# Kernel optimization log

Measured on AMD Instinct MI355X. Metric: run time of the kernel, lower is better.

Reference implementation:

```python
import jax, jax.numpy as jnp
import numpy as np

DN = ('NCHW', 'OIHW', 'NCHW')
B, H, W = 2048, 16, 16
DICT, SE, CE, ESZ, NZ = 14, 8, 16, 512, 512
EPS = 1e-4


def _conv(x, w, b):
    # 3x3 conv, padding=1 (SAME), NCHW
    return jax.lax.conv_general_dilated(x, w, (1, 1), 'SAME', dimension_numbers=DN) + b[None, :, None, None]


def _normalized(m, eps=0.0):
    return m / (jnp.sqrt(jnp.sum(m * m, axis=1, keepdims=True)) + eps)


def setup_inputs() -> dict:
    key = jax.random.key(0)
    ks = jax.random.split(key, 20)
    f = jnp.float32
    d = {
        's': jax.random.randint(ks[0], (B, H, W), 0, DICT, dtype=jnp.int32),
        's_prime': jax.random.randint(ks[1], (B, H, W), 0, DICT, dtype=jnp.int32),
        'state_embed': jax.random.normal(ks[2], (DICT, SE), f),
        'conv_embed_w': jax.random.normal(ks[3], (CE, SE, 3, 3), f) * 0.1,
        'conv_embed_b': jnp.zeros((CE,), f),
        'p1c1_w': jax.random.normal(ks[4], (16, CE, 3, 3), f) * 0.1,
        'p1c1_b': jnp.zeros((16,), f),
        'p1c2_w': jax.random.normal(ks[5], (32, 16, 3, 3), f) * 0.1,
        'p1c2_b': jnp.zeros((32,), f),
        'p1l_w': jax.random.normal(ks[6], (ESZ, 32 * H * W), f) * 0.02,
        'p1l_b': jnp.zeros((ESZ,), f),
        'p2c1_w': jax.random.normal(ks[7], (16, CE, 3, 3), f) * 0.1,
        'p2c1_b': jnp.zeros((16,), f),
        'p2c2_w': jax.random.normal(ks[8], (32, 16, 3, 3), f) * 0.1,
        'p2c2_b': jnp.zeros((32,), f),
        'p2l_w': jax.random.normal(ks[9], (ESZ, 32 * H * W), f) * 0.02,
        'p2l_b': jnp.zeros((ESZ,), f),
        'z_vectors': jax.random.normal(ks[10], (NZ, ESZ), f),
        'scale': jnp.ones((1,), f),
        'downscale_factor': 1,
    }
    return d


def _embed(s, state_embed, conv_embed_w, conv_embed_b):
    # nn.Embedding(max_norm=1): renorm rows to L2 norm <= 1 before lookup
    norms = jnp.sqrt(jnp.sum(state_embed * state_embed, axis=1, keepdims=True))
    table = state_embed / jnp.maximum(norms, 1.0)
    x = table[s]  # (B, H, W, SE)
    x = jnp.transpose(x, (0, 3, 1, 2))  # (B, SE, H, W)
    return _conv(x, conv_embed_w, conv_embed_b)


def _tower(x, c1w, c1b, c2w, c2b, lw, lb):
    x = jax.nn.relu(_conv(x, c1w, c1b))
    x = jax.nn.relu(_conv(x, c2w, c2b))
    x = x.reshape(x.shape[0], -1)  # (B, 32*H*W)
    x = x @ lw.T + lb
    return _normalized(x, EPS)


def reference(s, s_prime, state_embed, conv_embed_w, conv_embed_b,
              p1c1_w, p1c1_b, p1c2_w, p1c2_b, p1l_w, p1l_b,
              p2c1_w, p2c1_b, p2c2_w, p2c2_b, p2l_w, p2l_b,
              z_vectors, scale, downscale_factor):
    s_e = _embed(s, state_embed, conv_embed_w, conv_embed_b)
    sp_e = _embed(s_prime, state_embed, conv_embed_w, conv_embed_b)
    embed1 = _tower(s_e, p1c1_w, p1c1_b, p1c2_w, p1c2_b, p1l_w, p1l_b)
    embed2 = _tower(sp_e - s_e, p2c1_w, p2c1_b, p2c2_w, p2c2_b, p2l_w, p2l_b)
    # VQ: cosine-similarity nearest codebook vector
    zn = _normalized(z_vectors, 0.0)  # (NZ, ESZ)
    z_inds = jnp.argmax(embed2 @ zn.T, axis=1)  # (B,)
    z_matrix = zn[z_inds]  # (B, ESZ)
    if downscale_factor == 1:
        ipm = embed1 @ z_matrix.T  # (B, B)
    else:
        bs = embed1.shape[0] // downscale_factor
        v1 = embed1[::downscale_factor]  # (bs, ESZ)
        v2 = z_matrix.reshape(bs, downscale_factor, -1)
        ipm = jnp.einsum('be,bde->bd', v1, v2)
    return jnp.exp(scale) * ipm
```

## Files before the change

kernel.cpp:

```cpp
#include <hip/hip_runtime.h>
#include <math.h>


typedef __attribute__((ext_vector_type(8))) __bf16 bf16x8;
typedef __attribute__((ext_vector_type(4))) float f32x4;
typedef __attribute__((ext_vector_type(8))) unsigned short ushort8;
typedef __attribute__((ext_vector_type(4))) unsigned short ushort4v;

static __device__ __forceinline__ unsigned short f2bf(float x) {
  union { float f; unsigned u; } v; v.f = x;
  return (unsigned short)(v.u >> 16);
}
static __device__ __forceinline__ float bf2f(unsigned short h) {
  union { float f; unsigned u; } v; v.u = ((unsigned)h) << 16;
  return v.f;
}
template<int NS>
static __device__ __forceinline__ void split3(float x, unsigned short* h) {
  unsigned short q0 = f2bf(x); h[0] = q0;
  float r1 = x - bf2f(q0);
  unsigned short q1 = f2bf(r1); h[1] = q1;
  if constexpr (NS == 3) h[2] = f2bf(r1 - bf2f(q1));
}
static __device__ __forceinline__ void gload_lds16(const void* g, void* l) {
  __builtin_amdgcn_global_load_lds(
      (const __attribute__((address_space(1))) unsigned int*)g,
      (__attribute__((address_space(3))) unsigned int*)l, 16, 0, 0);
}
#define MFMA16(a, b, c) __builtin_amdgcn_mfma_f32_16x16x32_bf16((a), (b), (c), 0, 0, 0)

template<int NS>
static __device__ __forceinline__ f32x4 mfma_prod(const bf16x8* a, const bf16x8* b, f32x4 c) {
  c = MFMA16(a[0], b[0], c);
  c = MFMA16(a[0], b[1], c);
  c = MFMA16(a[1], b[0], c);
  if constexpr (NS == 3) {
    c = MFMA16(a[1], b[1], c);
    c = MFMA16(a[0], b[2], c);
    c = MFMA16(a[2], b[0], c);
  }
  return c;
}
static __device__ __forceinline__ int conv_a16(int cell, int half) {
  return (cell * 2 + half) ^ ((cell >> 2) & 7);
}
static __device__ __forceinline__ unsigned long long score_key(float v, int col) {
  unsigned b = __float_as_uint(v);
  unsigned m = b ^ ((unsigned)((int)b >> 31) | 0x80000000u);
  return ((unsigned long long)m << 32) | (unsigned)(511 - col);
}
static __device__ __forceinline__ unsigned long long shfl_xor_u64(unsigned long long v, int m) {
  unsigned lo = __shfl_xor((unsigned)v, m, 64);
  unsigned hi = __shfl_xor((unsigned)(v >> 32), m, 64);
  return ((unsigned long long)hi << 32) | lo;
}

__global__ __launch_bounds__(256) void prep_misc_kernel(
    const float* __restrict__ se, float* __restrict__ tbl,
    const float* __restrict__ zv,
    unsigned short* __restrict__ zn0, unsigned short* __restrict__ zn1,
    unsigned short* __restrict__ zn2,
    float* __restrict__ epre, unsigned long long* __restrict__ zi)
{
  __shared__ float wsum[4];
  const int b = blockIdx.x, t = threadIdx.x;
  if (b == 0) {
    if (t < 112) {
      int r = t >> 3;
      float ss = 0.f;
      #pragma unroll
      for (int i = 0; i < 8; ++i) { float v = se[r * 8 + i]; ss += v * v; }
      float n = fmaxf(sqrtf(ss), 1.0f);
      tbl[t] = se[t] / n;
    }
  } else if (b <= 512) {
    int row = b - 1;
    size_t base = (size_t)row * 512 + t * 2;
    float2 v = *reinterpret_cast<const float2*>(zv + base);
    float ss = v.x * v.x + v.y * v.y;
    #pragma unroll
    for (int m = 32; m >= 1; m >>= 1) ss += __shfl_xor(ss, m, 64);
    int lane = t & 63, wid = t >> 6;
    if (lane == 0) wsum[wid] = ss;
    __syncthreads();
    float tot = wsum[0] + wsum[1] + wsum[2] + wsum[3];
    float inv = 1.0f / sqrtf(tot);
    float a = v.x * inv, c = v.y * inv;
    unsigned short ha[3], hc[3];
    split3<3>(a, ha); split3<3>(c, hc);
    zn0[base] = ha[0]; zn0[base + 1] = hc[0];
    zn1[base] = ha[1]; zn1[base + 1] = hc[1];
    zn2[base] = ha[2]; zn2[base + 1] = hc[2];
  } else if (b <= 1024) {
    f32x4 z4 = {0.f, 0.f, 0.f, 0.f};
    size_t o = ((size_t)(b - 513) * 256 + t) * 8;
    *reinterpret_cast<f32x4*>(epre + o) = z4;
    *reinterpret_cast<f32x4*>(epre + o + 4) = z4;
  } else {
    int i = (b - 1025) * 256 + t;
    if (i < 2048) zi[i] = 0ull;
  }
}

__global__ __launch_bounds__(256) void prep_wt_all_kernel(
    const float* __restrict__ ew,
    const float* __restrict__ p1c1w, const float* __restrict__ p1c2w,
    const float* __restrict__ p2c1w, const float* __restrict__ p2c2w,
    unsigned short* __restrict__ wt)
{
  int gi = blockIdx.x * 256 + threadIdx.x;
  if (gi >= 50688) return;
  const float* src; int off, NSs, OC, mode;
  if (gi < 4608)       { src = ew;    off = 0;     NSs = 3; OC = 16; mode = 0; }
  else if (gi < 12288) { src = p1c1w; off = 4608;  NSs = 5; OC = 16; mode = 1; }
  else if (gi < 27648) { src = p1c2w; off = 12288; NSs = 5; OC = 32; mode = 1; }
  else if (gi < 35328) { src = p2c1w; off = 27648; NSs = 5; OC = 16; mode = 1; }
  else                 { src = p2c2w; off = 35328; NSs = 5; OC = 32; mode = 1; }
  int i = gi - off;
  int ic = i & 7;
  int r = i >> 3;
  int oc = r % OC; r /= OC;
  int kc = r & 3; r >>= 2;
  int s = r % NSs;
  int sp = r / NSs;
  int tap, icf, IC;
  if (mode == 0) { tap = s * 4 + kc; icf = ic; IC = 8; }
  else           { tap = s * 2 + (kc >> 1); icf = (kc & 1) * 8 + ic; IC = 16; }
  float w = 0.f;
  if (tap < 9) {
    int ky = tap / 3, kx = tap - ky * 3;
    w = src[((oc * IC + icf) * 3 + ky) * 3 + kx];
  }
  unsigned short h[3];
  split3<3>(w, h);
  wt[gi] = h[sp];
}

__global__ __launch_bounds__(256) void reduce_norm_kernel(
    const float* __restrict__ pre, const float* __restrict__ bias, float eps,
    unsigned short* __restrict__ o0, unsigned short* __restrict__ o1,
    unsigned short* __restrict__ o2, float* __restrict__ zero_dst)
{
  int row = blockIdx.x, t = threadIdx.x;
  size_t base = (size_t)row * 512 + t * 2;
  float2 v = *reinterpret_cast<const float2*>(pre + base);
  float ax = v.x + bias[t * 2], ay = v.y + bias[t * 2 + 1];
  float ss = ax * ax + ay * ay;
  #pragma unroll
  for (int m = 32; m >= 1; m >>= 1) ss += __shfl_xor(ss, m, 64);
  __shared__ float wsum[4];
  int lane = t & 63, wid = t >> 6;
  if (lane == 0) wsum[wid] = ss;
  __syncthreads();
  float tot = wsum[0] + wsum[1] + wsum[2] + wsum[3];
  float inv = 1.0f / (sqrtf(tot) + eps);
  float a = ax * inv, b2 = ay * inv;
  unsigned short ha[3], hb[3];
  split3<3>(a, ha); split3<3>(b2, hb);
  o0[base] = ha[0]; o0[base + 1] = hb[0];
  o1[base] = ha[1]; o1[base + 1] = hb[1];
  if (o2) { o2[base] = ha[2]; o2[base + 1] = hb[2]; }
  if (zero_dst) {
    float2 z = {0.f, 0.f};
    *reinterpret_cast<float2*>(zero_dst + base) = z;
  }
}

template<int NS>
__global__ __launch_bounds__(256) void tower_mfma_kernel(
    const int* __restrict__ sIdx, const int* __restrict__ spIdx,
    const float* __restrict__ tblf,
    const unsigned short* __restrict__ wtE,
    const unsigned short* __restrict__ wt1,
    const unsigned short* __restrict__ wt2,
    const float* __restrict__ eb, const float* __restrict__ c1b,
    const float* __restrict__ c2b,
    unsigned short* __restrict__ a0, unsigned short* __restrict__ a1,
    unsigned short* __restrict__ a2, int delta)
{
  __shared__ float tbl[112];
  __shared__ ushort8 G[NS][324];
  __shared__ ushort8 Abuf[NS][648];
  __shared__ ushort8 Bbuf[NS][648];

  const int b = blockIdx.x, t = threadIdx.x;
  const int lane = t & 63, wv = t >> 6;
  const int fr = lane & 15, kc = lane >> 4;

  if (t < 112) tbl[t] = tblf[t];
  if (t < 68) {
    int c;
    if (t < 18)      c = t;
    else if (t < 36) c = 306 + (t - 18);
    else if (t < 52) c = 18 * (t - 35);
    else             c = 18 * (t - 51) + 17;
    ushort8 z8 = {0, 0, 0, 0, 0, 0, 0, 0};
    #pragma unroll
    for (int sp = 0; sp < NS; ++sp) {
      G[sp][c] = z8;
      ((ushort8*)&Abuf[sp][0])[conv_a16(c, 0)] = z8;
      ((ushort8*)&Abuf[sp][0])[conv_a16(c, 1)] = z8;
      ((ushort8*)&Bbuf[sp][0])[conv_a16(c, 0)] = z8;
      ((ushort8*)&Bbuf[sp][0])[conv_a16(c, 1)] = z8;
    }
  }
  __syncthreads();

  {
    const int y = t >> 4, x = t & 15;
    const int cell = (y + 1) * 18 + (x + 1);
    int sv = sIdx[(size_t)b * 256 + t];
    float v[8];
    if (delta) {
      int spv = spIdx[(size_t)b * 256 + t];
      #pragma unroll
      for (int c = 0; c < 8; ++c) v[c] = tbl[spv * 8 + c] - tbl[sv * 8 + c];
    } else {
      #pragma unroll
      for (int c = 0; c < 8; ++c) v[c] = tbl[sv * 8 + c];
    }
    ushort8 h0, h1, h2;
    #pragma unroll
    for (int c = 0; c < 8; ++c) {
      unsigned short q[3];
      split3<NS>(v[c], q);
      h0[c] = q[0]; h1[c] = q[1];
      if constexpr (NS == 3) h2[c] = q[2];
    }
    G[0][cell] = h0; G[1][cell] = h1;
    if constexpr (NS == 3) G[2][cell] = h2;
  }
  __syncthreads();

  {
    float bias = 0.f;
    if (!delta) bias = eb[fr];
    f32x4 acc[4];
    #pragma unroll
    for (int j = 0; j < 4; ++j) acc[j] = (f32x4)0.f;
    #pragma unroll
    for (int s = 0; s < 3; ++s) {
      bf16x8 bw[NS];
      #pragma unroll
      for (int sp = 0; sp < NS; ++sp)
        bw[sp] = __builtin_bit_cast(bf16x8, *reinterpret_cast<const ushort8*>(
            wtE + (size_t)(((sp * 3 + s) * 4 + kc) * 16 + fr) * 8));
      int tap = s * 4 + kc; if (tap > 8) tap = 8;
      const int dy = tap / 3, dx = tap - dy * 3;
      const int cb = dy * 18 + fr + dx;
      #pragma unroll
      for (int j = 0; j < 4; ++j) {
        const int cell = cb + (wv * 4 + j) * 18;
        bf16x8 av[NS];
        #pragma unroll
        for (int sp = 0; sp < NS; ++sp)
          av[sp] = __builtin_bit_cast(bf16x8, G[sp][cell]);
        acc[j] = mfma_prod<NS>(av, bw, acc[j]);
      }
    }
    #pragma unroll
    for (int j = 0; j < 4; ++j) {
      const int y = wv * 4 + j;
      #pragma unroll
      for (int q = 0; q < 4; ++q) {
        const int x = kc * 4 + q;
        const int cell = (y + 1) * 18 + (x + 1);
        const int a16 = conv_a16(cell, fr >> 3);
        unsigned short hh[3];
        split3<NS>(acc[j][q] + bias, hh);
        #pragma unroll
        for (int sp = 0; sp < NS; ++sp)
          ((unsigned short*)&Abuf[sp][0])[a16 * 8 + (fr & 7)] = hh[sp];
      }
    }
  }
  __syncthreads();

  {
    const float bias = c1b[fr];
    f32x4 acc[4];
    #pragma unroll
    for (int j = 0; j < 4; ++j) acc[j] = (f32x4)0.f;
    #pragma unroll
    for (int s = 0; s < 5; ++s) {
      bf16x8 bw[NS];
      #pragma unroll
      for (int sp = 0; sp < NS; ++sp)
        bw[sp] = __builtin_bit_cast(bf16x8, *reinterpret_cast<const ushort8*>(
            wt1 + (size_t)(((sp * 5 + s) * 4 + kc) * 16 + fr) * 8));
      int tap = s * 2 + (kc >> 1); if (tap > 8) tap = 8;
      const int dy = tap / 3, dx = tap - dy * 3;
      const int half = kc & 1;
      const int cb = dy * 18 + fr + dx;
      #pragma unroll
      for (int j = 0; j < 4; ++j) {
        const int cell = cb + (wv * 4 + j) * 18;
        const int a16 = conv_a16(cell, half);
        bf16x8 av[NS];
        #pragma unroll
        for (int sp = 0; sp < NS; ++sp)
          av[sp] = __builtin_bit_cast(bf16x8, *reinterpret_cast<const ushort8*>(
              (const unsigned short*)&Abuf[sp][0] + a16 * 8));
        acc[j] = mfma_prod<NS>(av, bw, acc[j]);
      }
    }
    #pragma unroll
    for (int j = 0; j < 4; ++j) {
      const int y = wv * 4 + j;
      #pragma unroll
      for (int q = 0; q < 4; ++q) {
        const int x = kc * 4 + q;
        const int cell = (y + 1) * 18 + (x + 1);
        const int a16 = conv_a16(cell, fr >> 3);
        unsigned short hh[3];
        split3<NS>(fmaxf(acc[j][q] + bias, 0.f), hh);
        #pragma unroll
        for (int sp = 0; sp < NS; ++sp)
          ((unsigned short*)&Bbuf[sp][0])[a16 * 8 + (fr & 7)] = hh[sp];
      }
    }
  }
  __syncthreads();

  {
    const float bias0 = c2b[fr], bias1 = c2b[16 + fr];
    f32x4 acc0[4], acc1[4];
    #pragma unroll
    for (int j = 0; j < 4; ++j) { acc0[j] = (f32x4)0.f; acc1[j] = (f32x4)0.f; }
    #pragma unroll
    for (int s = 0; s < 5; ++s) {
      bf16x8 bw0[NS], bw1[NS];
      #pragma unroll
      for (int sp = 0; sp < NS; ++sp) {
        size_t base = (size_t)(((sp * 5 + s) * 4 + kc) * 32) * 8;
        bw0[sp] = __builtin_bit_cast(bf16x8,
            *reinterpret_cast<const ushort8*>(wt2 + base + (size_t)fr * 8));
        bw1[sp] = __builtin_bit_cast(bf16x8,
            *reinterpret_cast<const ushort8*>(wt2 + base + (size_t)(16 + fr) * 8));
      }
      int tap = s * 2 + (kc >> 1); if (tap > 8) tap = 8;
      const int dy = tap / 3, dx = tap - dy * 3;
      const int half = kc & 1;
      const int cb = dy * 18 + fr + dx;
      #pragma unroll
      for (int j = 0; j < 4; ++j) {
        const int cell = cb + (wv * 4 + j) * 18;
        const int a16 = conv_a16(cell, half);
        bf16x8 av[NS];
        #pragma unroll
        for (int sp = 0; sp < NS; ++sp)
          av[sp] = __builtin_bit_cast(bf16x8, *reinterpret_cast<const ushort8*>(
              (const unsigned short*)&Bbuf[sp][0] + a16 * 8));
        acc0[j] = mfma_prod<NS>(av, bw0, acc0[j]);
        acc1[j] = mfma_prod<NS>(av, bw1, acc1[j]);
      }
    }
    #pragma unroll
    for (int j = 0; j < 4; ++j) {
      const int y = wv * 4 + j;
      ushort4v g0[2], g1[2], g2[2];
      #pragma unroll
      for (int q = 0; q < 4; ++q) {
        unsigned short hh[3];
        split3<NS>(fmaxf(acc0[j][q] + bias0, 0.f), hh);
        g0[0][q] = hh[0]; g1[0][q] = hh[1]; if constexpr (NS == 3) g2[0][q] = hh[2];
        split3<NS>(fmaxf(acc1[j][q] + bias1, 0.f), hh);
        g0[1][q] = hh[0]; g1[1][q] = hh[1]; if constexpr (NS == 3) g2[1][q] = hh[2];
      }
      size_t base0 = (size_t)b * 8192 + (size_t)fr * 256 + y * 16 + kc * 4;
      size_t base1 = base0 + 16 * 256;
      *reinterpret_cast<ushort4v*>(a0 + base0) = g0[0];
      *reinterpret_cast<ushort4v*>(a0 + base1) = g0[1];
      *reinterpret_cast<ushort4v*>(a1 + base0) = g1[0];
      *reinterpret_cast<ushort4v*>(a1 + base1) = g1[1];
      if constexpr (NS == 3) {
        *reinterpret_cast<ushort4v*>(a2 + base0) = g2[0];
        *reinterpret_cast<ushort4v*>(a2 + base1) = g2[1];
      }
    }
  }
}

template<int NS, bool BF32, int EPI>
__global__ __launch_bounds__(256) void mfma_gemm_kernel(
    const unsigned short* __restrict__ A0, const unsigned short* __restrict__ A1,
    const unsigned short* __restrict__ A2,
    const unsigned short* __restrict__ B0, const unsigned short* __restrict__ B1,
    const unsigned short* __restrict__ B2,
    const float* __restrict__ Bf32,
    const unsigned long long* __restrict__ gkey,
    unsigned long long* __restrict__ zout,
    const float* __restrict__ scale_p,
    float* __restrict__ C, int M, int N, int K, int Ksub)
{
  __shared__ unsigned short ldsA[NS][4096];
  __shared__ unsigned short ldsB[NS][4096];

  const int t = threadIdx.x;
  const int lane = t & 63, wv = t >> 6;
  const int m0 = blockIdx.x * 128, n0 = blockIdx.y * 128;
  const long kbase = (long)blockIdx.z * Ksub;
  const int NT = Ksub >> 5;

  const int st_row = lane >> 2;
  const int st_cb = (lane & 3) * 16;
  int srow[2];
  long bgrow[2];
  #pragma unroll
  for (int r = 0; r < 2; ++r) {
    srow[r] = (wv + 4 * r) * 16 + st_row;
    if constexpr (!BF32) {
      long g = n0 + srow[r];
      if constexpr (EPI == 2)
        g = 511 - (long)(unsigned)(gkey[n0 + srow[r]] & 0xFFFFFFFFull);
      bgrow[r] = g;
    }
  }

  const int wr = wv >> 1, wc = wv & 1;
  const int fr = lane & 15, kc = lane >> 4;

  f32x4 acc[4][4];
  #pragma unroll
  for (int mi = 0; mi < 4; ++mi)
    #pragma unroll
    for (int ni = 0; ni < 4; ++ni) acc[mi][ni] = (f32x4)0.f;

  const unsigned short* Asp[3] = {A0, A1, A2};
  const unsigned short* Bsp[3] = {B0, B1, B2};

  for (int kt = 0; kt < NT; ++kt) {
    const long k0 = kbase + (long)kt * 32;
    #pragma unroll
    for (int sp = 0; sp < NS; ++sp)
      #pragma unroll
      for (int r = 0; r < 2; ++r) {
        int row = srow[r];
        int c = st_cb ^ (((row >> 1) & 3) << 4);
        gload_lds16(Asp[sp] + (size_t)(m0 + row) * K + k0 + (c >> 1),
                    &ldsA[sp][(wv + 4 * r) * 512]);
      }
    if constexpr (BF32) {
      #pragma unroll
      for (int i = 0; i < 4; ++i) {
        int row = (t >> 3) + 32 * i;
        f32x4 v = *reinterpret_cast<const f32x4*>(
            Bf32 + (size_t)(n0 + row) * K + k0 + (t & 7) * 4);
        int cb = ((t & 7) * 8) ^ (((row >> 1) & 3) << 4);
        ushort4v w0, w1, w2;
        #pragma unroll
        for (int jj = 0; jj < 4; ++jj) {
          unsigned short hh[3];
          split3<NS>(v[jj], hh);
          w0[jj] = hh[0]; w1[jj] = hh[1];
          if constexpr (NS == 3) w2[jj] = hh[2];
        }
        *reinterpret_cast<ushort4v*>(&ldsB[0][row * 32 + (cb >> 1)]) = w0;
        *reinterpret_cast<ushort4v*>(&ldsB[1][row * 32 + (cb >> 1)]) = w1;
        if constexpr (NS == 3)
          *reinterpret_cast<ushort4v*>(&ldsB[2][row * 32 + (cb >> 1)]) = w2;
      }
    } else {
      #pragma unroll
      for (int sp = 0; sp < NS; ++sp)
        #pragma unroll
        for (int r = 0; r < 2; ++r) {
          int row = srow[r];
          int c = st_cb ^ (((row >> 1) & 3) << 4);
          gload_lds16(Bsp[sp] + (size_t)bgrow[r] * K + k0 + (c >> 1),
                      &ldsB[sp][(wv + 4 * r) * 512]);
        }
    }
    __syncthreads();

    bf16x8 af[NS][4], bf[NS][4];
    #pragma unroll
    for (int sp = 0; sp < NS; ++sp) {
      #pragma unroll
      for (int mi = 0; mi < 4; ++mi) {
        int row = wr * 64 + mi * 16 + fr;
        int cb = (kc * 16) ^ (((row >> 1) & 3) << 4);
        af[sp][mi] = __builtin_bit_cast(bf16x8,
            *reinterpret_cast<const ushort8*>(&ldsA[sp][row * 32 + (cb >> 1)]));
      }
      #pragma unroll
      for (int ni = 0; ni < 4; ++ni) {
        int row = wc * 64 + ni * 16 + fr;
        int cb = (kc * 16) ^ (((row >> 1) & 3) << 4);
        bf[sp][ni] = __builtin_bit_cast(bf16x8,
            *reinterpret_cast<const ushort8*>(&ldsB[sp][row * 32 + (cb >> 1)]));
      }
    }
    #pragma unroll
    for (int mi = 0; mi < 4; ++mi)
      #pragma unroll
      for (int ni = 0; ni < 4; ++ni) {
        f32x4 c = acc[mi][ni];
        c = MFMA16(af[0][mi], bf[0][ni], c);
        c = MFMA16(af[0][mi], bf[1][ni], c);
        c = MFMA16(af[1][mi], bf[0][ni], c);
        if constexpr (NS == 3) {
          c = MFMA16(af[1][mi], bf[1][ni], c);
          c = MFMA16(af[0][mi], bf[2][ni], c);
          c = MFMA16(af[2][mi], bf[0][ni], c);
        }
        acc[mi][ni] = c;
      }
    __syncthreads();
  }

  if constexpr (EPI == 0) {
    #pragma unroll
    for (int mi = 0; mi < 4; ++mi)
      #pragma unroll
      for (int ni = 0; ni < 4; ++ni) {
        int col = n0 + wc * 64 + ni * 16 + fr;
        #pragma unroll
        for (int q = 0; q < 4; ++q) {
          int row = m0 + wr * 64 + mi * 16 + kc * 4 + q;
          atomicAdd(&C[(size_t)row * N + col], acc[mi][ni][q]);
        }
      }
  } else if constexpr (EPI == 2) {
    float scl = expf(scale_p[0]);
    #pragma unroll
    for (int mi = 0; mi < 4; ++mi)
      #pragma unroll
      for (int ni = 0; ni < 4; ++ni) {
        int col = n0 + wc * 64 + ni * 16 + fr;
        #pragma unroll
        for (int q = 0; q < 4; ++q) {
          int row = m0 + wr * 64 + mi * 16 + kc * 4 + q;
          C[(size_t)row * N + col] = acc[mi][ni][q] * scl;
        }
      }
  } else {
    #pragma unroll
    for (int mi = 0; mi < 4; ++mi)
      #pragma unroll
      for (int q = 0; q < 4; ++q) {
        int row = m0 + wr * 64 + mi * 16 + kc * 4 + q;
        unsigned long long best = 0ull;
        #pragma unroll
        for (int ni = 0; ni < 4; ++ni) {
          int col = n0 + wc * 64 + ni * 16 + fr;
          unsigned long long k2 = score_key(acc[mi][ni][q], col);
          best = (k2 > best) ? k2 : best;
        }
        #pragma unroll
        for (int m2 = 1; m2 < 16; m2 <<= 1) {
          unsigned long long o = shfl_xor_u64(best, m2);
          best = (o > best) ? o : best;
        }
        if (fr == 0) atomicMax(zout + row, best);
      }
  }
}

extern "C" void kernel_launch(void* const* d_in, const int* in_sizes, int n_in,
                              void* d_out, int out_size, void* d_ws, size_t ws_size,
                              hipStream_t stream)
{
  const int*   s      = (const int*)  d_in[0];
  const int*   sprime = (const int*)  d_in[1];
  const float* se     = (const float*)d_in[2];
  const float* ew     = (const float*)d_in[3];
  const float* eb     = (const float*)d_in[4];
  const float* p1c1w  = (const float*)d_in[5];
  const float* p1c1b  = (const float*)d_in[6];
  const float* p1c2w  = (const float*)d_in[7];
  const float* p1c2b  = (const float*)d_in[8];
  const float* p1lw   = (const float*)d_in[9];
  const float* p1lb   = (const float*)d_in[10];
  const float* p2c1w  = (const float*)d_in[11];
  const float* p2c1b  = (const float*)d_in[12];
  const float* p2c2w  = (const float*)d_in[13];
  const float* p2c2b  = (const float*)d_in[14];
  const float* p2lw   = (const float*)d_in[15];
  const float* p2lb   = (const float*)d_in[16];
  const float* zv     = (const float*)d_in[17];
  const float* scale  = (const float*)d_in[18];
  float* out = (float*)d_out;

  char* w = (char*)d_ws;
  size_t off = 0;
  auto alloc = [&](size_t bytes) -> char* {
    char* p = w + off;
    off += (bytes + 255) & ~(size_t)255;
    return p;
  };
  float* tblf = (float*)alloc(112 * 4);
  unsigned short* zn0 = (unsigned short*)alloc((size_t)512 * 512 * 2);
  unsigned short* zn1 = (unsigned short*)alloc((size_t)512 * 512 * 2);
  unsigned short* zn2 = (unsigned short*)alloc((size_t)512 * 512 * 2);
  unsigned short* e10 = (unsigned short*)alloc((size_t)2048 * 512 * 2);
  unsigned short* e11 = (unsigned short*)alloc((size_t)2048 * 512 * 2);
  unsigned short* e20 = (unsigned short*)alloc((size_t)2048 * 512 * 2);
  unsigned short* e21 = (unsigned short*)alloc((size_t)2048 * 512 * 2);
  unsigned short* e22 = (unsigned short*)alloc((size_t)2048 * 512 * 2);
  float* epre = (float*)alloc((size_t)2048 * 512 * 4);
  unsigned long long* zi = (unsigned long long*)alloc(2048 * 8);
  unsigned short* wt = (unsigned short*)alloc((size_t)50688 * 2);
  unsigned short* act0 = (unsigned short*)alloc((size_t)2048 * 8192 * 2);
  unsigned short* act1 = (unsigned short*)alloc((size_t)2048 * 8192 * 2);
  unsigned short* act2 = (unsigned short*)alloc((size_t)2048 * 8192 * 2);

  unsigned short* wtE  = wt;
  unsigned short* wt1a = wt + 4608;
  unsigned short* wt2a = wt + 12288;
  unsigned short* wt1b = wt + 27648;
  unsigned short* wt2b = wt + 35328;

  prep_misc_kernel<<<1033, 256, 0, stream>>>(se, tblf, zv, zn0, zn1, zn2, epre, zi);
  prep_wt_all_kernel<<<198, 256, 0, stream>>>(ew, p1c1w, p1c2w, p2c1w, p2c2w, wt);

  tower_mfma_kernel<2><<<2048, 256, 0, stream>>>(
      s, sprime, tblf, wtE, wt1a, wt2a, eb, p1c1b, p1c2b, act0, act1, act2, 0);
  mfma_gemm_kernel<2, true, 0><<<dim3(16, 4, 16), 256, 0, stream>>>(
      act0, act1, nullptr, nullptr, nullptr, nullptr, p1lw, nullptr, nullptr,
      nullptr, epre, 2048, 512, 8192, 512);
  reduce_norm_kernel<<<2048, 256, 0, stream>>>(epre, p1lb, 1e-4f,
                                               e10, e11, nullptr, epre);

  tower_mfma_kernel<3><<<2048, 256, 0, stream>>>(
      s, sprime, tblf, wtE, wt1b, wt2b, eb, p2c1b, p2c2b, act0, act1, act2, 1);
  mfma_gemm_kernel<3, true, 0><<<dim3(16, 4, 16), 256, 0, stream>>>(
      act0, act1, act2, nullptr, nullptr, nullptr, p2lw, nullptr, nullptr,
      nullptr, epre, 2048, 512, 8192, 512);
  reduce_norm_kernel<<<2048, 256, 0, stream>>>(epre, p2lb, 1e-4f,
                                               e20, e21, e22, nullptr);

  mfma_gemm_kernel<3, false, 3><<<dim3(16, 4, 1), 256, 0, stream>>>(
      e20, e21, e22, zn0, zn1, zn2, nullptr, nullptr, zi, nullptr,
      nullptr, 2048, 512, 512, 512);
  mfma_gemm_kernel<2, false, 2><<<dim3(16, 16, 1), 256, 0, stream>>>(
      e10, e11, nullptr, zn0, zn1, nullptr, nullptr, zi, nullptr, scale,
      out, 2048, 2048, 512, 512);
}
```

Baseline: 502.7 us.

## Pre-split linear weights to bf16 planes once instead of per GEMM tile

Adds a kernel that splits the fp32 linear-layer weights into bf16 hi/lo planes, two planes for tower 1 and three for tower 2, before the towers run. The big GEMMs then load B with async global-to-LDS copies like A, instead of reading fp32 and splitting it inside every tile (16 M-blocks each redid that work). The split-K factor also drops from 16 to 8, halving atomic/partial accumulation traffic but launching fewer blocks. The change adds an extra pass over the weights and reuses part of act2 as scratch for the tower-1 planes, which is safe only because tower 1 does not write act2.

```diff
diff --git a/kernel.cpp b/kernel.cpp
--- a/kernel.cpp
+++ b/kernel.cpp
@@ -136,6 +136,41 @@
   wt[gi] = h[sp];
 }
 
+__global__ __launch_bounds__(256) void split_lin_kernel(
+    const float* __restrict__ p1, const float* __restrict__ p2,
+    unsigned short* __restrict__ w0, unsigned short* __restrict__ w1,
+    unsigned short* __restrict__ u0, unsigned short* __restrict__ u1,
+    unsigned short* __restrict__ u2)
+{
+  int blk = blockIdx.x;
+  if (blk < 4096) {
+    size_t i = ((size_t)blk * 256 + threadIdx.x) * 4;
+    f32x4 v = *reinterpret_cast<const f32x4*>(p1 + i);
+    ushort4v a, b;
+    #pragma unroll
+    for (int j = 0; j < 4; ++j) {
+      unsigned short h[3];
+      split3<2>(v[j], h);
+      a[j] = h[0]; b[j] = h[1];
+    }
+    *reinterpret_cast<ushort4v*>(w0 + i) = a;
+    *reinterpret_cast<ushort4v*>(w1 + i) = b;
+  } else {
+    size_t i = ((size_t)(blk - 4096) * 256 + threadIdx.x) * 4;
+    f32x4 v = *reinterpret_cast<const f32x4*>(p2 + i);
+    ushort4v a, b, c;
+    #pragma unroll
+    for (int j = 0; j < 4; ++j) {
+      unsigned short h[3];
+      split3<3>(v[j], h);
+      a[j] = h[0]; b[j] = h[1]; c[j] = h[2];
+    }
+    *reinterpret_cast<ushort4v*>(u0 + i) = a;
+    *reinterpret_cast<ushort4v*>(u1 + i) = b;
+    *reinterpret_cast<ushort4v*>(u2 + i) = c;
+  }
+}
+
 __global__ __launch_bounds__(256) void reduce_norm_kernel(
     const float* __restrict__ pre, const float* __restrict__ bias, float eps,
     unsigned short* __restrict__ o0, unsigned short* __restrict__ o1,
@@ -381,13 +416,12 @@
   }
 }
 
-template<int NS, bool BF32, int EPI>
+template<int NS, int EPI>
 __global__ __launch_bounds__(256) void mfma_gemm_kernel(
     const unsigned short* __restrict__ A0, const unsigned short* __restrict__ A1,
     const unsigned short* __restrict__ A2,
     const unsigned short* __restrict__ B0, const unsigned short* __restrict__ B1,
     const unsigned short* __restrict__ B2,
-    const float* __restrict__ Bf32,
     const unsigned long long* __restrict__ gkey,
     unsigned long long* __restrict__ zout,
     const float* __restrict__ scale_p,
@@ -409,12 +443,10 @@
   #pragma unroll
   for (int r = 0; r < 2; ++r) {
     srow[r] = (wv + 4 * r) * 16 + st_row;
-    if constexpr (!BF32) {
-      long g = n0 + srow[r];
-      if constexpr (EPI == 2)
-        g = 511 - (long)(unsigned)(gkey[n0 + srow[r]] & 0xFFFFFFFFull);
-      bgrow[r] = g;
-    }
+    long g = n0 + srow[r];
+    if constexpr (EPI == 2)
+      g = 511 - (long)(unsigned)(gkey[n0 + srow[r]] & 0xFFFFFFFFull);
+    bgrow[r] = g;
   }
 
   const int wr = wv >> 1, wc = wv & 1;
@@ -440,37 +472,15 @@
         gload_lds16(Asp[sp] + (size_t)(m0 + row) * K + k0 + (c >> 1),
                     &ldsA[sp][(wv + 4 * r) * 512]);
       }
-    if constexpr (BF32) {
-      #pragma unroll
-      for (int i = 0; i < 4; ++i) {
-        int row = (t >> 3) + 32 * i;
-        f32x4 v = *reinterpret_cast<const f32x4*>(
-            Bf32 + (size_t)(n0 + row) * K + k0 + (t & 7) * 4);
-        int cb = ((t & 7) * 8) ^ (((row >> 1) & 3) << 4);
-        ushort4v w0, w1, w2;
-        #pragma unroll
-        for (int jj = 0; jj < 4; ++jj) {
-          unsigned short hh[3];
-          split3<NS>(v[jj], hh);
-          w0[jj] = hh[0]; w1[jj] = hh[1];
-          if constexpr (NS == 3) w2[jj] = hh[2];
-        }
-        *reinterpret_cast<ushort4v*>(&ldsB[0][row * 32 + (cb >> 1)]) = w0;
-        *reinterpret_cast<ushort4v*>(&ldsB[1][row * 32 + (cb >> 1)]) = w1;
-        if constexpr (NS == 3)
-          *reinterpret_cast<ushort4v*>(&ldsB[2][row * 32 + (cb >> 1)]) = w2;
-      }
-    } else {
-      #pragma unroll
-      for (int sp = 0; sp < NS; ++sp)
-        #pragma unroll
-        for (int r = 0; r < 2; ++r) {
-          int row = srow[r];
-          int c = st_cb ^ (((row >> 1) & 3) << 4);
-          gload_lds16(Bsp[sp] + (size_t)bgrow[r] * K + k0 + (c >> 1),
-                      &ldsB[sp][(wv + 4 * r) * 512]);
-        }
-    }
+    #pragma unroll
+    for (int sp = 0; sp < NS; ++sp)
+      #pragma unroll
+      for (int r = 0; r < 2; ++r) {
+        int row = srow[r];
+        int c = st_cb ^ (((row >> 1) & 3) << 4);
+        gload_lds16(Bsp[sp] + (size_t)bgrow[r] * K + k0 + (c >> 1),
+                    &ldsB[sp][(wv + 4 * r) * 512]);
+      }
     __syncthreads();
 
     bf16x8 af[NS][4], bf[NS][4];
@@ -604,6 +614,11 @@
   unsigned short* act0 = (unsigned short*)alloc((size_t)2048 * 8192 * 2);
   unsigned short* act1 = (unsigned short*)alloc((size_t)2048 * 8192 * 2);
   unsigned short* act2 = (unsigned short*)alloc((size_t)2048 * 8192 * 2);
+  unsigned short* u0 = (unsigned short*)alloc((size_t)512 * 8192 * 2);
+  unsigned short* u1 = (unsigned short*)alloc((size_t)512 * 8192 * 2);
+  unsigned short* u2 = (unsigned short*)alloc((size_t)512 * 8192 * 2);
+  unsigned short* w0 = act2;
+  unsigned short* w1 = act2 + (size_t)512 * 8192;
 
   unsigned short* wtE  = wt;
   unsigned short* wt1a = wt + 4608;
@@ -613,27 +628,28 @@
 
   prep_misc_kernel<<<1033, 256, 0, stream>>>(se, tblf, zv, zn0, zn1, zn2, epre, zi);
   prep_wt_all_kernel<<<198, 256, 0, stream>>>(ew, p1c1w, p1c2w, p2c1w, p2c2w, wt);
+  split_lin_kernel<<<8192, 256, 0, stream>>>(p1lw, p2lw, w0, w1, u0, u1, u2);
 
   tower_mfma_kernel<2><<<2048, 256, 0, stream>>>(
       s, sprime, tblf, wtE, wt1a, wt2a, eb, p1c1b, p1c2b, act0, act1, act2, 0);
-  mfma_gemm_kernel<2, true, 0><<<dim3(16, 4, 16), 256, 0, stream>>>(
-      act0, act1, nullptr, nullptr, nullptr, nullptr, p1lw, nullptr, nullptr,
-      nullptr, epre, 2048, 512, 8192, 512);
+  mfma_gemm_kernel<2, 0><<<dim3(16, 4, 8), 256, 0, stream>>>(
+      act0, act1, nullptr, w0, w1, nullptr, nullptr, nullptr,
+      nullptr, epre, 2048, 512, 8192, 1024);
   reduce_norm_kernel<<<2048, 256, 0, stream>>>(epre, p1lb, 1e-4f,
                                                e10, e11, nullptr, epre);
 
   tower_mfma_kernel<3><<<2048, 256, 0, stream>>>(
       s, sprime, tblf, wtE, wt1b, wt2b, eb, p2c1b, p2c2b, act0, act1, act2, 1);
-  mfma_gemm_kernel<3, true, 0><<<dim3(16, 4, 16), 256, 0, stream>>>(
-      act0, act1, act2, nullptr, nullptr, nullptr, p2lw, nullptr, nullptr,
-      nullptr, epre, 2048, 512, 8192, 512);
+  mfma_gemm_kernel<3, 0><<<dim3(16, 4, 8), 256, 0, stream>>>(
+      act0, act1, act2, u0, u1, u2, nullptr, nullptr,
+      nullptr, epre, 2048, 512, 8192, 1024);
   reduce_norm_kernel<<<2048, 256, 0, stream>>>(epre, p2lb, 1e-4f,
                                                e20, e21, e22, nullptr);
 
-  mfma_gemm_kernel<3, false, 3><<<dim3(16, 4, 1), 256, 0, stream>>>(
-      e20, e21, e22, zn0, zn1, zn2, nullptr, nullptr, zi, nullptr,
+  mfma_gemm_kernel<3, 3><<<dim3(16, 4, 1), 256, 0, stream>>>(
+      e20, e21, e22, zn0, zn1, zn2, nullptr, zi, nullptr,
       nullptr, 2048, 512, 512, 512);
-  mfma_gemm_kernel<2, false, 2><<<dim3(16, 16, 1), 256, 0, stream>>>(
-      e10, e11, nullptr, zn0, zn1, nullptr, nullptr, zi, nullptr, scale,
+  mfma_gemm_kernel<2, 2><<<dim3(16, 16, 1), 256, 0, stream>>>(
+      e10, e11, nullptr, zn0, zn1, nullptr, zi, nullptr, scale,
       out, 2048, 2048, 512, 512);
 }
```

New measurement: 474.1 us. -5.7%, faster.
